# Performance work log

Hardware: AMD Instinct MI355X
Metric: run time of the kernel (lower is better)

## Reference

```python
import jax, jax.numpy as jnp
import numpy as np

N = 8192       # number of nodes (dense NxN attention)
F_IN = 256     # input feature dim
F_OUT = 64     # projected feature dim (F_prime)
NEG_SLOPE = 0.01  # nn.LeakyReLU default


def setup_inputs() -> dict:
    key = jax.random.key(0)
    k0, k1, k2, k3 = jax.random.split(key, 4)
    H = jax.random.normal(k0, (N, F_IN), dtype=jnp.float32)
    # dense 0/1 adjacency; force self-loops so every row has a nonzero denominator
    A = jax.random.randint(k1, (N, N), 0, 2, dtype=jnp.int32)
    A = jnp.maximum(A, jnp.eye(N, dtype=jnp.int32))
    # learned params: W : F_IN -> F_OUT (self.W), a : 2*F_OUT -> 1 (self.a)
    W = jax.random.normal(k2, (F_IN, F_OUT), dtype=jnp.float32) / np.sqrt(F_IN)
    bW = jnp.zeros((F_OUT,), dtype=jnp.float32)
    a_w = jax.random.normal(k3, (2 * F_OUT,), dtype=jnp.float32) / np.sqrt(2 * F_OUT)
    a_b = jnp.zeros((), dtype=jnp.float32)
    return {"H": H, "A": A, "W": W, "bW": bW, "a_w": a_w, "a_b": a_b}


def reference(H, A, W, bW, a_w, a_b):
    # Wh[i] = W(H[i])  -> [N, F_OUT]
    Wh = H @ W + bW
    # a([Wh_i ; Wh_j]) = a1.Wh_i + a2.Wh_j + a_b : decompose the concat-linear
    s_src = Wh @ a_w[:F_OUT]           # [N]
    s_tar = Wh @ a_w[F_OUT:]           # [N]
    logits = s_src[:, None] + s_tar[None, :] + a_b   # [N, N]
    # e_ij = exp(leaky_relu(logits))
    e = jnp.exp(jnp.where(logits >= 0, logits, NEG_SLOPE * logits))
    # denominator masks by adjacency (sum_j e_ij * A_ij), as in the original
    denom = jnp.sum(e * A.astype(e.dtype), axis=1, keepdims=True)  # [N, 1]
    alpha = e / denom                   # NOTE: numerator NOT masked (faithful)
    # H'_i = sigmoid(alpha_i @ Wh)
    return jax.nn.sigmoid(alpha @ Wh)   # [N, F_OUT]
```

## Files before the change

kernel.cpp:

```cpp
#include <hip/hip_runtime.h>
#include <hip/hip_bf16.h>

#define NN 8192
#define FIN 256
#define FOUT 64

typedef int iv4 __attribute__((ext_vector_type(4)));

__global__ __launch_bounds__(256) void k1_proj(
    const float* __restrict__ H, const float* __restrict__ W,
    const float* __restrict__ bW, const float* __restrict__ aw,
    const float* __restrict__ ab,
    float* __restrict__ Wh, float* __restrict__ s_src, float* __restrict__ t_tar,
    float* __restrict__ E1, float* __restrict__ E2, float* __restrict__ PP)
{
    __shared__ float Hs[16 * FIN];
    int tid = threadIdx.x;
    int i0 = blockIdx.x * 16;
    const float4* Hv = (const float4*)(H + (size_t)i0 * FIN);
    float4* Hsv = (float4*)Hs;
    for (int idx = tid; idx < 16 * FIN / 4; idx += 256) Hsv[idx] = Hv[idx];
    __syncthreads();
    int f = tid & 63, sub = tid >> 6;
    float a1f = aw[f], a2f = aw[64 + f];
    float b = bW[f];
    float acc0 = b, acc1 = b, acc2 = b, acc3 = b;
    for (int k = 0; k < FIN; ++k) {
        float w = W[k * FOUT + f];
        acc0 += Hs[(sub     ) * FIN + k] * w;
        acc1 += Hs[(sub +  4) * FIN + k] * w;
        acc2 += Hs[(sub +  8) * FIN + k] * w;
        acc3 += Hs[(sub + 12) * FIN + k] * w;
    }
    float accs[4] = {acc0, acc1, acc2, acc3};
    #pragma unroll
    for (int q = 0; q < 4; ++q) {
        int i = i0 + sub + 4 * q;
        float a = accs[q];
        Wh[(size_t)i * FOUT + f] = a;
        float v1 = a * a1f, v2 = a * a2f;
        #pragma unroll
        for (int o = 32; o > 0; o >>= 1) {
            v1 += __shfl_xor(v1, o);
            v2 += __shfl_xor(v2, o);
        }
        if (f == 0) {
            float s = v1 + ab[0];
            float t = v2;
            s_src[i] = s; t_tar[i] = t;
            E1[i] = __expf(s); E2[i] = __expf(0.01f * s);
            PP[2 * i]     = __expf(t);
            PP[2 * i + 1] = __expf(0.01f * t);
        }
    }
}

__global__ __launch_bounds__(256) void k2_rank(
    const float* __restrict__ t_tar, const float* __restrict__ s_src,
    int* __restrict__ sorted_idx, int* __restrict__ kidx)
{
    __shared__ float Ts[NN];
    int tid = threadIdx.x;
    const float4* tv = (const float4*)t_tar;
    float4* Tsv = (float4*)Ts;
    for (int idx = tid; idx < NN / 4; idx += 256) Tsv[idx] = tv[idx];
    __syncthreads();
    int wv = tid >> 6, lane = tid & 63;
    int gA = blockIdx.x * 8 + wv * 2;
    int gB = gA + 1;
    float tjA = Ts[gA], tjB = Ts[gB];
    float thrA = -s_src[gA], thrB = -s_src[gB];
    int rA = 0, kA = 0, rB = 0, kB = 0;
    #pragma unroll 4
    for (int k = lane; k < NN; k += 64) {
        float tk = Ts[k];
        rA += (tk < tjA || (tk == tjA && k < gA)) ? 1 : 0;
        kA += (tk < thrA) ? 1 : 0;
        rB += (tk < tjB || (tk == tjB && k < gB)) ? 1 : 0;
        kB += (tk < thrB) ? 1 : 0;
    }
    #pragma unroll
    for (int o = 32; o > 0; o >>= 1) {
        rA += __shfl_xor(rA, o); kA += __shfl_xor(kA, o);
        rB += __shfl_xor(rB, o); kB += __shfl_xor(kB, o);
    }
    if (lane == 0) {
        sorted_idx[rA] = gA; kidx[gA] = kA;
        sorted_idx[rB] = gB; kidx[gB] = kB;
    }
}

__global__ __launch_bounds__(64) void k3a_tots(
    const float* __restrict__ Wh, const float* __restrict__ PP,
    const int* __restrict__ sorted_idx,
    float* __restrict__ tots1, float* __restrict__ tots2)
{
    int c = blockIdx.x, f = threadIdx.x;
    float t1 = 0.f, t2 = 0.f;
    int m0 = c * 32;
    #pragma unroll 8
    for (int m = m0; m < m0 + 32; ++m) {
        int sj = sorted_idx[m];
        float wh = Wh[(size_t)sj * 64 + f];
        t1 += PP[2 * sj]     * wh;
        t2 += PP[2 * sj + 1] * wh;
    }
    tots1[c * 64 + f] = t1; tots2[c * 64 + f] = t2;
}

__global__ __launch_bounds__(64) void k3bc_emit(
    const float* __restrict__ Wh, const float* __restrict__ PP,
    const int* __restrict__ sorted_idx,
    const float* __restrict__ tots1, const float* __restrict__ tots2,
    float* __restrict__ pre2, float* __restrict__ suf1)
{
    int c = blockIdx.x, f = threadIdx.x;
    float o2 = 0.f;
    #pragma unroll 8
    for (int w = 0; w < c; ++w) o2 += tots2[w * 64 + f];
    float o1 = 0.f;
    #pragma unroll 8
    for (int w = c + 1; w < 256; ++w) o1 += tots1[w * 64 + f];
    int m0 = c * 32;
    float whr[32], p1r[32], p2r[32];
    #pragma unroll
    for (int q = 0; q < 32; ++q) {
        int sj = sorted_idx[m0 + q];
        whr[q] = Wh[(size_t)sj * 64 + f];
        p1r[q] = PP[2 * sj]; p2r[q] = PP[2 * sj + 1];
    }
    float run2 = o2;
    #pragma unroll
    for (int q = 0; q < 32; ++q) {
        pre2[(size_t)(m0 + q) * 64 + f] = run2;
        run2 += p2r[q] * whr[q];
    }
    if (c == 255) pre2[(size_t)NN * 64 + f] = run2;
    float run1 = o1;
    #pragma unroll
    for (int q = 31; q >= 0; --q) {
        run1 += p1r[q] * whr[q];
        suf1[(size_t)(m0 + q) * 64 + f] = run1;
    }
    if (c == 255) suf1[(size_t)NN * 64 + f] = 0.f;
}

__global__ __launch_bounds__(256) void k45_denom_out(
    const int* __restrict__ A, const float* __restrict__ PP,
    const float* __restrict__ E1, const float* __restrict__ E2,
    const float* __restrict__ suf1, const float* __restrict__ pre2,
    const int* __restrict__ kidx, float* __restrict__ out)
{
    int tid = threadIdx.x;
    int i0 = blockIdx.x * 8;
    float e1r[8], accA[8], accB[8];
    #pragma unroll
    for (int r = 0; r < 8; ++r) { e1r[r] = E1[i0 + r]; accA[r] = 0.f; accB[r] = 0.f; }
    const float4* PPv = (const float4*)PP;
    for (int jv = tid; jv < NN / 4; jv += 256) {
        float4 ppA = PPv[2 * jv];
        float4 ppB = PPv[2 * jv + 1];
        #pragma unroll
        for (int r = 0; r < 8; ++r) {
            const iv4 a4 = __builtin_nontemporal_load(
                (const iv4*)(A + (size_t)(i0 + r) * NN + jv * 4));
            float e1 = e1r[r];
            {
                bool c = e1 * ppA.x >= 1.0f;
                float af = (float)a4.x;
                accA[r] += af * (c ? ppA.x : 0.0f);
                accB[r] += af * (c ? 0.0f : ppA.y);
            }
            {
                bool c = e1 * ppA.z >= 1.0f;
                float af = (float)a4.y;
                accA[r] += af * (c ? ppA.z : 0.0f);
                accB[r] += af * (c ? 0.0f : ppA.w);
            }
            {
                bool c = e1 * ppB.x >= 1.0f;
                float af = (float)a4.z;
                accA[r] += af * (c ? ppB.x : 0.0f);
                accB[r] += af * (c ? 0.0f : ppB.y);
            }
            {
                bool c = e1 * ppB.z >= 1.0f;
                float af = (float)a4.w;
                accA[r] += af * (c ? ppB.z : 0.0f);
                accB[r] += af * (c ? 0.0f : ppB.w);
            }
        }
    }
    #pragma unroll
    for (int r = 0; r < 8; ++r) {
        #pragma unroll
        for (int o = 32; o > 0; o >>= 1) {
            accA[r] += __shfl_xor(accA[r], o);
            accB[r] += __shfl_xor(accB[r], o);
        }
    }
    __shared__ float red[4][8][2];
    __shared__ float sden[8];
    int wv = tid >> 6;
    if ((tid & 63) == 0) {
        #pragma unroll
        for (int r = 0; r < 8; ++r) { red[wv][r][0] = accA[r]; red[wv][r][1] = accB[r]; }
    }
    __syncthreads();
    if (tid < 8) {
        float sA = red[0][tid][0] + red[1][tid][0] + red[2][tid][0] + red[3][tid][0];
        float sB = red[0][tid][1] + red[1][tid][1] + red[2][tid][1] + red[3][tid][1];
        sden[tid] = E1[i0 + tid] * sA + E2[i0 + tid] * sB;
    }
    __syncthreads();
    int f = tid & 63, sub = tid >> 6;
    #pragma unroll
    for (int rr = 0; rr < 2; ++rr) {
        int r = sub + 4 * rr;
        int i = i0 + r;
        int k = kidx[i];
        float num = E1[i] * suf1[(size_t)k * 64 + f] + E2[i] * pre2[(size_t)k * 64 + f];
        float x = num / sden[r];
        out[(size_t)i * 64 + f] = 1.0f / (1.0f + __expf(-x));
    }
}

extern "C" void kernel_launch(void* const* d_in, const int* in_sizes, int n_in,
                              void* d_out, int out_size, void* d_ws, size_t ws_size,
                              hipStream_t stream) {
    const float* H  = (const float*)d_in[0];
    const int*   A  = (const int*)d_in[1];
    const float* W  = (const float*)d_in[2];
    const float* bW = (const float*)d_in[3];
    const float* aw = (const float*)d_in[4];
    const float* ab = (const float*)d_in[5];
    float* out = (float*)d_out;

    float* ws    = (float*)d_ws;
    float* Wh    = ws;
    float* s_src = Wh + 524288;
    float* t_tar = s_src + 8192;
    float* E1    = t_tar + 8192;
    float* E2    = E1 + 8192;
    float* PP    = E2 + 8192;
    float* pre2  = PP + 16384;
    float* suf1  = pre2 + 524352;
    float* tots1 = suf1 + 524352;
    float* tots2 = tots1 + 16384;
    int* sorted_idx = (int*)(tots2 + 16384);
    int* kidx       = sorted_idx + 8192;

    hipLaunchKernelGGL(k1_proj, dim3(512), dim3(256), 0, stream,
                       H, W, bW, aw, ab, Wh, s_src, t_tar, E1, E2, PP);
    hipLaunchKernelGGL(k2_rank, dim3(1024), dim3(256), 0, stream,
                       t_tar, s_src, sorted_idx, kidx);
    hipLaunchKernelGGL(k3a_tots, dim3(256), dim3(64), 0, stream,
                       Wh, PP, sorted_idx, tots1, tots2);
    hipLaunchKernelGGL(k3bc_emit, dim3(256), dim3(64), 0, stream,
                       Wh, PP, sorted_idx, tots1, tots2, pre2, suf1);
    hipLaunchKernelGGL(k45_denom_out, dim3(1024), dim3(256), 0, stream,
                       A, PP, E1, E2, suf1, pre2, kidx, out);
}
```

Before: 409.7 us.

## Fuse rank computation with adjacency denominator pass using atomic work-stealing

Merges the ranking kernel and the adjacency-masked denominator reduction into one launch. The first 256 blocks compute ranks (8 nodes per wave instead of 2), and all blocks then pull 8-row denominator units from an atomic counter, so the A-streaming work overlaps the rank phase instead of waiting for it. The output sigmoid is split into a small separate kernel that reads a stored denominator array. This adds an atomic counter, reset in the projection kernel, and a dependency on work-stealing balance.

```diff
diff --git a/kernel.cpp b/kernel.cpp
--- a/kernel.cpp
+++ b/kernel.cpp
@@ -1,9 +1,11 @@
 #include <hip/hip_runtime.h>
-#include <hip/hip_bf16.h>
 
 #define NN 8192
 #define FIN 256
 #define FOUT 64
+#define NRANK 256
+#define NBLK 1024
+#define NUNITS 1024
 
 typedef int iv4 __attribute__((ext_vector_type(4)));
 
@@ -12,10 +14,12 @@
     const float* __restrict__ bW, const float* __restrict__ aw,
     const float* __restrict__ ab,
     float* __restrict__ Wh, float* __restrict__ s_src, float* __restrict__ t_tar,
-    float* __restrict__ E1, float* __restrict__ E2, float* __restrict__ PP)
+    float* __restrict__ E1, float* __restrict__ E2, float* __restrict__ PP,
+    unsigned* __restrict__ ctrs)
 {
     __shared__ float Hs[16 * FIN];
     int tid = threadIdx.x;
+    if (blockIdx.x == 0 && tid < 4) ctrs[tid] = 0u;
     int i0 = blockIdx.x * 16;
     const float4* Hv = (const float4*)(H + (size_t)i0 * FIN);
     float4* Hsv = (float4*)Hs;
@@ -55,38 +59,123 @@
     }
 }
 
-__global__ __launch_bounds__(256) void k2_rank(
+__global__ __launch_bounds__(256, 4) void kA_rank_denom(
+    const int* __restrict__ A,
     const float* __restrict__ t_tar, const float* __restrict__ s_src,
-    int* __restrict__ sorted_idx, int* __restrict__ kidx)
+    const float* __restrict__ PP,
+    const float* __restrict__ E1, const float* __restrict__ E2,
+    int* __restrict__ sorted_idx, int* __restrict__ kidx,
+    float* __restrict__ denom, unsigned* __restrict__ ctrs)
 {
     __shared__ float Ts[NN];
-    int tid = threadIdx.x;
-    const float4* tv = (const float4*)t_tar;
-    float4* Tsv = (float4*)Ts;
-    for (int idx = tid; idx < NN / 4; idx += 256) Tsv[idx] = tv[idx];
-    __syncthreads();
-    int wv = tid >> 6, lane = tid & 63;
-    int gA = blockIdx.x * 8 + wv * 2;
-    int gB = gA + 1;
-    float tjA = Ts[gA], tjB = Ts[gB];
-    float thrA = -s_src[gA], thrB = -s_src[gB];
-    int rA = 0, kA = 0, rB = 0, kB = 0;
-    #pragma unroll 4
-    for (int k = lane; k < NN; k += 64) {
-        float tk = Ts[k];
-        rA += (tk < tjA || (tk == tjA && k < gA)) ? 1 : 0;
-        kA += (tk < thrA) ? 1 : 0;
-        rB += (tk < tjB || (tk == tjB && k < gB)) ? 1 : 0;
-        kB += (tk < thrB) ? 1 : 0;
-    }
-    #pragma unroll
-    for (int o = 32; o > 0; o >>= 1) {
-        rA += __shfl_xor(rA, o); kA += __shfl_xor(kA, o);
-        rB += __shfl_xor(rB, o); kB += __shfl_xor(kB, o);
-    }
-    if (lane == 0) {
-        sorted_idx[rA] = gA; kidx[gA] = kA;
-        sorted_idx[rB] = gB; kidx[gB] = kB;
+    __shared__ float red[4][8][2];
+    __shared__ unsigned ucur;
+    int tid = threadIdx.x, wv = tid >> 6, lane = tid & 63;
+    int b = blockIdx.x;
+
+    if (b < NRANK) {
+        const float4* tv = (const float4*)t_tar;
+        float4* Tsv = (float4*)Ts;
+        for (int idx = tid; idx < NN / 4; idx += 256) Tsv[idx] = tv[idx];
+        __syncthreads();
+        int g0 = b * 32 + wv * 8;
+        float tj[8], thr[8];
+        int rk[8], kc[8];
+        #pragma unroll
+        for (int q = 0; q < 8; ++q) {
+            tj[q] = Ts[g0 + q];
+            thr[q] = -s_src[g0 + q];
+            rk[q] = 0; kc[q] = 0;
+        }
+        for (int k = lane; k < NN; k += 64) {
+            float tk = Ts[k];
+            #pragma unroll
+            for (int q = 0; q < 8; ++q) {
+                rk[q] += (tk < tj[q] || (tk == tj[q] && k < g0 + q)) ? 1 : 0;
+                kc[q] += (tk < thr[q]) ? 1 : 0;
+            }
+        }
+        #pragma unroll
+        for (int q = 0; q < 8; ++q) {
+            #pragma unroll
+            for (int o = 32; o > 0; o >>= 1) {
+                rk[q] += __shfl_xor(rk[q], o);
+                kc[q] += __shfl_xor(kc[q], o);
+            }
+        }
+        if (lane == 0) {
+            #pragma unroll
+            for (int q = 0; q < 8; ++q) {
+                sorted_idx[rk[q]] = g0 + q;
+                kidx[g0 + q] = kc[q];
+            }
+        }
+    }
+
+    for (;;) {
+        if (tid == 0) ucur = atomicAdd(&ctrs[0], 1u);
+        __syncthreads();
+        unsigned u = ucur;
+        __syncthreads();
+        if (u >= NUNITS) break;
+        int i0 = (int)u * 8;
+        float e1r[8], accA[8], accB[8];
+        #pragma unroll
+        for (int r = 0; r < 8; ++r) { e1r[r] = E1[i0 + r]; accA[r] = 0.f; accB[r] = 0.f; }
+        const float4* PPv = (const float4*)PP;
+        for (int jv = tid; jv < NN / 4; jv += 256) {
+            float4 ppA = PPv[2 * jv];
+            float4 ppB = PPv[2 * jv + 1];
+            #pragma unroll
+            for (int r = 0; r < 8; ++r) {
+                const iv4 a4 = __builtin_nontemporal_load(
+                    (const iv4*)(A + (size_t)(i0 + r) * NN + jv * 4));
+                float e1 = e1r[r];
+                {
+                    bool c = e1 * ppA.x >= 1.0f;
+                    float af = (float)a4.x;
+                    accA[r] += af * (c ? ppA.x : 0.0f);
+                    accB[r] += af * (c ? 0.0f : ppA.y);
+                }
+                {
+                    bool c = e1 * ppA.z >= 1.0f;
+                    float af = (float)a4.y;
+                    accA[r] += af * (c ? ppA.z : 0.0f);
+                    accB[r] += af * (c ? 0.0f : ppA.w);
+                }
+                {
+                    bool c = e1 * ppB.x >= 1.0f;
+                    float af = (float)a4.z;
+                    accA[r] += af * (c ? ppB.x : 0.0f);
+                    accB[r] += af * (c ? 0.0f : ppB.y);
+                }
+                {
+                    bool c = e1 * ppB.z >= 1.0f;
+                    float af = (float)a4.w;
+                    accA[r] += af * (c ? ppB.z : 0.0f);
+                    accB[r] += af * (c ? 0.0f : ppB.w);
+                }
+            }
+        }
+        #pragma unroll
+        for (int r = 0; r < 8; ++r) {
+            #pragma unroll
+            for (int o = 32; o > 0; o >>= 1) {
+                accA[r] += __shfl_xor(accA[r], o);
+                accB[r] += __shfl_xor(accB[r], o);
+            }
+        }
+        if ((tid & 63) == 0) {
+            #pragma unroll
+            for (int r = 0; r < 8; ++r) { red[wv][r][0] = accA[r]; red[wv][r][1] = accB[r]; }
+        }
+        __syncthreads();
+        if (tid < 8) {
+            float sA = red[0][tid][0] + red[1][tid][0] + red[2][tid][0] + red[3][tid][0];
+            float sB = red[0][tid][1] + red[1][tid][1] + red[2][tid][1] + red[3][tid][1];
+            denom[i0 + tid] = E1[i0 + tid] * sA + E2[i0 + tid] * sB;
+        }
+        __syncthreads();
     }
 }
 
@@ -145,84 +234,19 @@
     if (c == 255) suf1[(size_t)NN * 64 + f] = 0.f;
 }
 
-__global__ __launch_bounds__(256) void k45_denom_out(
-    const int* __restrict__ A, const float* __restrict__ PP,
-    const float* __restrict__ E1, const float* __restrict__ E2,
+__global__ __launch_bounds__(256) void k5_out(
     const float* __restrict__ suf1, const float* __restrict__ pre2,
-    const int* __restrict__ kidx, float* __restrict__ out)
+    const int* __restrict__ kidx, const float* __restrict__ E1,
+    const float* __restrict__ E2, const float* __restrict__ denom,
+    float* __restrict__ out)
 {
     int tid = threadIdx.x;
-    int i0 = blockIdx.x * 8;
-    float e1r[8], accA[8], accB[8];
-    #pragma unroll
-    for (int r = 0; r < 8; ++r) { e1r[r] = E1[i0 + r]; accA[r] = 0.f; accB[r] = 0.f; }
-    const float4* PPv = (const float4*)PP;
-    for (int jv = tid; jv < NN / 4; jv += 256) {
-        float4 ppA = PPv[2 * jv];
-        float4 ppB = PPv[2 * jv + 1];
-        #pragma unroll
-        for (int r = 0; r < 8; ++r) {
-            const iv4 a4 = __builtin_nontemporal_load(
-                (const iv4*)(A + (size_t)(i0 + r) * NN + jv * 4));
-            float e1 = e1r[r];
-            {
-                bool c = e1 * ppA.x >= 1.0f;
-                float af = (float)a4.x;
-                accA[r] += af * (c ? ppA.x : 0.0f);
-                accB[r] += af * (c ? 0.0f : ppA.y);
-            }
-            {
-                bool c = e1 * ppA.z >= 1.0f;
-                float af = (float)a4.y;
-                accA[r] += af * (c ? ppA.z : 0.0f);
-                accB[r] += af * (c ? 0.0f : ppA.w);
-            }
-            {
-                bool c = e1 * ppB.x >= 1.0f;
-                float af = (float)a4.z;
-                accA[r] += af * (c ? ppB.x : 0.0f);
-                accB[r] += af * (c ? 0.0f : ppB.y);
-            }
-            {
-                bool c = e1 * ppB.z >= 1.0f;
-                float af = (float)a4.w;
-                accA[r] += af * (c ? ppB.z : 0.0f);
-                accB[r] += af * (c ? 0.0f : ppB.w);
-            }
-        }
-    }
-    #pragma unroll
-    for (int r = 0; r < 8; ++r) {
-        #pragma unroll
-        for (int o = 32; o > 0; o >>= 1) {
-            accA[r] += __shfl_xor(accA[r], o);
-            accB[r] += __shfl_xor(accB[r], o);
-        }
-    }
-    __shared__ float red[4][8][2];
-    __shared__ float sden[8];
-    int wv = tid >> 6;
-    if ((tid & 63) == 0) {
-        #pragma unroll
-        for (int r = 0; r < 8; ++r) { red[wv][r][0] = accA[r]; red[wv][r][1] = accB[r]; }
-    }
-    __syncthreads();
-    if (tid < 8) {
-        float sA = red[0][tid][0] + red[1][tid][0] + red[2][tid][0] + red[3][tid][0];
-        float sB = red[0][tid][1] + red[1][tid][1] + red[2][tid][1] + red[3][tid][1];
-        sden[tid] = E1[i0 + tid] * sA + E2[i0 + tid] * sB;
-    }
-    __syncthreads();
     int f = tid & 63, sub = tid >> 6;
-    #pragma unroll
-    for (int rr = 0; rr < 2; ++rr) {
-        int r = sub + 4 * rr;
-        int i = i0 + r;
-        int k = kidx[i];
-        float num = E1[i] * suf1[(size_t)k * 64 + f] + E2[i] * pre2[(size_t)k * 64 + f];
-        float x = num / sden[r];
-        out[(size_t)i * 64 + f] = 1.0f / (1.0f + __expf(-x));
-    }
+    int i = blockIdx.x * 4 + sub;
+    int k = kidx[i];
+    float num = E1[i] * suf1[(size_t)k * 64 + f] + E2[i] * pre2[(size_t)k * 64 + f];
+    float x = num / denom[i];
+    out[(size_t)i * 64 + f] = 1.0f / (1.0f + __expf(-x));
 }
 
 extern "C" void kernel_launch(void* const* d_in, const int* in_sizes, int n_in,
@@ -247,17 +271,19 @@
     float* suf1  = pre2 + 524352;
     float* tots1 = suf1 + 524352;
     float* tots2 = tots1 + 16384;
-    int* sorted_idx = (int*)(tots2 + 16384);
+    float* denom = tots2 + 16384;
+    int* sorted_idx = (int*)(denom + 8192);
     int* kidx       = sorted_idx + 8192;
+    unsigned* ctrs  = (unsigned*)(kidx + 8192);
 
     hipLaunchKernelGGL(k1_proj, dim3(512), dim3(256), 0, stream,
-                       H, W, bW, aw, ab, Wh, s_src, t_tar, E1, E2, PP);
-    hipLaunchKernelGGL(k2_rank, dim3(1024), dim3(256), 0, stream,
-                       t_tar, s_src, sorted_idx, kidx);
+                       H, W, bW, aw, ab, Wh, s_src, t_tar, E1, E2, PP, ctrs);
+    hipLaunchKernelGGL(kA_rank_denom, dim3(NBLK), dim3(256), 0, stream,
+                       A, t_tar, s_src, PP, E1, E2, sorted_idx, kidx, denom, ctrs);
     hipLaunchKernelGGL(k3a_tots, dim3(256), dim3(64), 0, stream,
                        Wh, PP, sorted_idx, tots1, tots2);
     hipLaunchKernelGGL(k3bc_emit, dim3(256), dim3(64), 0, stream,
                        Wh, PP, sorted_idx, tots1, tots2, pre2, suf1);
-    hipLaunchKernelGGL(k45_denom_out, dim3(1024), dim3(256), 0, stream,
-                       A, PP, E1, E2, suf1, pre2, kidx, out);
-}
+    hipLaunchKernelGGL(k5_out, dim3(2048), dim3(256), 0, stream,
+                       suf1, pre2, kidx, E1, E2, denom, out);
+}
```

Measured after the change: 409.3 us. About the same (-0.1%).
